# Kernel optimization log

Hardware: AMD Instinct MI355X
Metric: run time of the kernel (lower is better)

## Reference

```python
import jax, jax.numpy as jnp
import numpy as np

B, N, D, V, Y = 4, 2048, 300, 50000, 20000
MAX_REL = 10
LN_EPS = 1e-5


def setup_inputs() -> dict:
    key = jax.random.key(0)
    k1, k2, k3, k4, k5 = jax.random.split(key, 5)
    M_s = jax.random.randint(k1, (B, N), 0, V, dtype=jnp.int64)
    s = 1.0 / np.sqrt(D)
    E_v = jax.random.normal(k2, (V, D), dtype=jnp.float32) * s
    E_v = E_v.at[0].set(0.0)  # padding_idx=0
    E_y = jax.random.normal(k3, (Y, D), dtype=jnp.float32) * s
    E_y = E_y.at[0].set(0.0)
    W_A = jax.random.normal(k4, (D, D), dtype=jnp.float32) * s
    W_O = jax.random.normal(k5, (D, D), dtype=jnp.float32) * s
    gamma = jnp.ones((D,), dtype=jnp.float32)
    beta = jnp.zeros((D,), dtype=jnp.float32)
    return {"M_s": M_s, "E_v": E_v, "E_y": E_y, "W_A": W_A, "W_O": W_O,
            "gamma": gamma, "beta": beta}


def reference(M_s, E_v, E_y, W_A, W_O, gamma, beta):
    # Embedding lookup (dropout is identity in eval / p=0)
    X = E_v[M_s]                                   # [B, N, D]
    Q = X                                          # self-attention mode (v_q=None)
    # weights = Q @ W_A @ X^T
    QW = jnp.einsum('bnd,de->bne', Q, W_A)         # [B, N, D]
    weights = jnp.einsum('bne,bme->bnm', QW, X)    # [B, N, N]
    # relative-distance bias (clipped |i-j|)
    r = jnp.arange(N)
    dist = jnp.clip(jnp.abs(r[None, :] - r[:, None]), 0, MAX_REL).astype(weights.dtype)
    weights = weights - dist
    # padding mask over context (key) positions
    mask = (M_s != 0)                              # [B, N]
    weights = jnp.where(mask[:, None, :], weights, -jnp.inf)
    A = jax.nn.softmax(weights, axis=-1)           # [B, N, N]
    # contextualized query + output projection
    Q_c = jnp.einsum('bnm,bmd->bnd', A, X) @ W_O   # [B, N, D]
    # residual + layernorm over D
    H = Q_c + Q
    mu = jnp.mean(H, axis=-1, keepdims=True)
    var = jnp.mean((H - mu) ** 2, axis=-1, keepdims=True)
    Hn = (H - mu) * jax.lax.rsqrt(var + LN_EPS) * gamma + beta
    # vocab projection over senses
    y_logits = Hn @ E_y.T                          # [B, N, Y]
    return y_logits, A
```

## Files before the change

### kernel.cpp

```cpp
#include <hip/hip_runtime.h>
#include <hip/hip_bf16.h>

#define B_ 4
#define N_ 2048
#define D_ 300
#define Y_ 20000
#define ROWS (B_*N_)

typedef __attribute__((ext_vector_type(8))) short bf16x8;
typedef __attribute__((ext_vector_type(4))) float f32x4;

__device__ __forceinline__ unsigned short f2bf(float f) {
  unsigned u = __float_as_uint(f);
  unsigned r = (u + 0x7FFFu + ((u >> 16) & 1u)) >> 16;
  return (unsigned short)r;
}

__device__ __forceinline__ void gl_lds16(const unsigned short* g, unsigned short* l) {
  __builtin_amdgcn_global_load_lds(
      (const __attribute__((address_space(1))) void*)g,
      (__attribute__((address_space(3))) void*)l, 16, 0, 0);
}

__global__ __launch_bounds__(256) void k_gather_pack(const int* __restrict__ M_s,
    const float* __restrict__ E_v, float* __restrict__ X,
    unsigned short* __restrict__ Xp) {
  __shared__ float xs[320];
  int row = blockIdx.x, tid = threadIdx.x;
  int tok = M_s[row];
  const float* src = E_v + (size_t)tok * D_;
  for (int d = tid; d < 320; d += 256) xs[d] = (d < D_) ? src[d] : 0.f;
  __syncthreads();
  float* dst = X + (size_t)row * D_;
  for (int d = tid; d < D_; d += 256) dst[d] = xs[d];
  if (tid < 40) {
    int kt = tid >> 2, j = tid & 3;
    int tile = row >> 7, fb = (row >> 4) & 7, rl = row & 15;
    unsigned short v[8];
    #pragma unroll
    for (int e = 0; e < 8; ++e) v[e] = f2bf(xs[kt*32 + j*8 + e]);
    size_t off_ = ((size_t)(tile*10 + kt))*4096 + fb*512 + rl*8 + j*128;
    ushort4* o = (ushort4*)&Xp[off_];
    o[0] = make_ushort4(v[0],v[1],v[2],v[3]);
    o[1] = make_ushort4(v[4],v[5],v[6],v[7]);
  }
}

__global__ __launch_bounds__(256) void k_pack(const float* __restrict__ src,
    unsigned short* __restrict__ dst, int nrows, int ncols, int KT) {
  int chunk = blockIdx.x;
  int tile = chunk / KT, kt = chunk - tile*KT;
  size_t obase = (size_t)chunk * 4096;
  #pragma unroll
  for (int p = 0; p < 2; ++p) {
    int idx = p*256 + threadIdx.x;
    int fb = idx >> 6, l = idx & 63;
    int row = tile*128 + fb*16 + (l & 15);
    int gk = kt*32 + (l >> 4)*8;
    unsigned short v[8];
    #pragma unroll
    for (int e = 0; e < 8; ++e) {
      int k = gk + e;
      float f = (row < nrows && k < ncols) ? src[(size_t)row*ncols + k] : 0.f;
      v[e] = f2bf(f);
    }
    ushort4* o = (ushort4*)&dst[obase + (size_t)idx*8];
    o[0] = make_ushort4(v[0],v[1],v[2],v[3]);
    o[1] = make_ushort4(v[4],v[5],v[6],v[7]);
  }
}

__global__ __launch_bounds__(256) void k_packT(const float* __restrict__ src,
    unsigned short* __restrict__ dst, int src_rows, int src_cols, int KT,
    size_t src_bstride, size_t dst_bchunks) {
  __shared__ float ls[32*133];
  int chunk = blockIdx.x, b = blockIdx.y, tid = threadIdx.x;
  const float* s = src + (size_t)b * src_bstride;
  unsigned short* d = dst + ((size_t)b * dst_bchunks + chunk) * 4096;
  int tile = chunk / KT, kt = chunk - tile*KT;
  int c0 = tile*128, k0 = kt*32;
  for (int i = tid; i < 4096; i += 256) {
    int r = i >> 7, c = i & 127;
    int sr = k0 + r, sc = c0 + c;
    ls[r*133 + c] = (sr < src_rows && sc < src_cols) ? s[(size_t)sr*src_cols + sc] : 0.f;
  }
  __syncthreads();
  #pragma unroll
  for (int p = 0; p < 2; ++p) {
    int idx = p*256 + tid;
    int fb = idx >> 6, l = idx & 63;
    int r = fb*16 + (l & 15);
    int kl = (l >> 4)*8;
    unsigned short v[8];
    #pragma unroll
    for (int e = 0; e < 8; ++e) v[e] = f2bf(ls[(kl + e)*133 + r]);
    ushort4* o = (ushort4*)&d[(size_t)idx*8];
    o[0] = make_ushort4(v[0],v[1],v[2],v[3]);
    o[1] = make_ushort4(v[4],v[5],v[6],v[7]);
  }
}

template<int EPI, bool NT, bool PACKOUT, bool SWZ>
__global__ __launch_bounds__(256) void k_gemm10(
    const unsigned short* __restrict__ Ap, const unsigned short* __restrict__ Bp,
    float* __restrict__ out, unsigned short* __restrict__ outp,
    const float* __restrict__ resid, const int* __restrict__ Ms,
    int KTd, int MTB, int NTB, int ncols)
{
  __shared__ __align__(16) union {
    unsigned short bstage[10][4096];
    float epi[64*132];
  } sm;
  int nt, mt, z;
  if (SWZ) {
    int nwg = MTB * NTB;
    int wg = blockIdx.x;
    int cpx = nwg >> 3;
    int swz = (wg & 7) * cpx + (wg >> 3);
    mt = swz % MTB; nt = swz / MTB; z = 0;
  } else {
    nt = blockIdx.x; mt = blockIdx.y; z = blockIdx.z;
  }
  const int tid = threadIdx.x;
  const int wave = tid >> 6, lane = tid & 63;
  const int wm = wave >> 1, wn = wave & 1;
  const unsigned short* Ab = Ap + (size_t)(z*MTB + mt) * 10 * 4096;
  const unsigned short* Bb = Bp + (size_t)(z*NTB + nt) * 10 * 4096;

  #pragma unroll
  for (int kt = 0; kt < 10; ++kt) {
    const unsigned short* gb = Bb + kt*4096 + wave*1024 + lane*8;
    unsigned short* lb = &sm.bstage[kt][wave*1024];
    gl_lds16(gb,       lb);
    gl_lds16(gb + 512, lb + 512);
  }

  const unsigned short* ga = Ab + (wm*4)*512 + lane*8;
  bf16x8 aA[4], aB[4];
  #pragma unroll
  for (int i = 0; i < 4; ++i) aA[i] = *(const bf16x8*)(ga + 0*4096 + i*512);
  #pragma unroll
  for (int i = 0; i < 4; ++i) aB[i] = *(const bf16x8*)(ga + 1*4096 + i*512);

  __syncthreads();

  f32x4 acc[4][4] = {};
  auto mfma_step = [&](int kt, const bf16x8* a) {
    bf16x8 bfr[4];
    #pragma unroll
    for (int i = 0; i < 4; ++i)
      bfr[i] = *(const bf16x8*)&sm.bstage[kt][(wn*4 + i)*512 + lane*8];
    #pragma unroll
    for (int mi = 0; mi < 4; ++mi)
      #pragma unroll
      for (int ni = 0; ni < 4; ++ni)
        acc[mi][ni] = __builtin_amdgcn_mfma_f32_16x16x32_bf16(
            a[mi], bfr[ni], acc[mi][ni], 0, 0, 0);
  };
  auto loadA = [&](int kt, bf16x8* d) {
    #pragma unroll
    for (int i = 0; i < 4; ++i) d[i] = *(const bf16x8*)(ga + kt*4096 + i*512);
  };

  #pragma unroll
  for (int kt = 0; kt < 10; kt += 2) {
    mfma_step(kt, aA);
    if (kt + 2 < 10) loadA(kt + 2, aA);
    mfma_step(kt + 1, aB);
    if (kt + 3 < 10) loadA(kt + 3, aB);
  }

  __syncthreads();

  const int lr0 = (lane >> 4) << 2;
  const int lc0 = wn*64 + (lane & 15);
  const size_t growbase = ((size_t)(z*MTB + mt)) << 7;
  #pragma unroll
  for (int h = 0; h < 2; ++h) {
    if (wm == h) {
      int tok[4];
      if (EPI == 1) {
        #pragma unroll
        for (int ni = 0; ni < 4; ++ni)
          tok[ni] = Ms[z*N_ + (nt<<7) + lc0 + ni*16];
      }
      #pragma unroll
      for (int mi = 0; mi < 4; ++mi) {
        #pragma unroll
        for (int ni = 0; ni < 4; ++ni) {
          int col = lc0 + ni*16;
          #pragma unroll
          for (int r = 0; r < 4; ++r) {
            int row = lr0 + mi*16 + r;
            float v = acc[mi][ni][r];
            if (EPI == 1) {
              int rb = (mt<<7) + h*64 + row;
              int gc = (nt<<7) + col;
              int dd = rb - gc; if (dd < 0) dd = -dd; if (dd > 10) dd = 10;
              v -= (float)dd;
              if (tok[ni] == 0) v = -3.0e38f;
            }
            sm.epi[row*132 + col] = v;
          }
        }
      }
    }
    __syncthreads();
    if (PACKOUT) {
      int prow = tid >> 2, pktq = tid & 3;
      int ktd = nt*4 + pktq;
      if (ktd < KTd) {
        int grl = h*64 + prow;
        int fb = grl >> 4, rl = grl & 15;
        size_t cbase = ((size_t)((z*MTB + mt)*KTd + ktd))*4096 + fb*512 + rl*8;
        #pragma unroll
        for (int oct = 0; oct < 4; ++oct) {
          unsigned short v[8];
          #pragma unroll
          for (int e = 0; e < 8; ++e)
            v[e] = f2bf(sm.epi[prow*132 + pktq*32 + oct*8 + e]);
          ushort4* o = (ushort4*)&outp[cbase + oct*128];
          o[0] = make_ushort4(v[0],v[1],v[2],v[3]);
          o[1] = make_ushort4(v[4],v[5],v[6],v[7]);
        }
      }
    } else {
      const int r0 = tid >> 5;
      const int c4 = (tid & 31) << 2;
      const int gc = (nt << 7) + c4;
      #pragma unroll
      for (int rr = r0; rr < 64; rr += 8) {
        size_t grow = growbase + h*64 + rr;
        if (gc + 3 < ncols) {
          f32x4 v = *(const f32x4*)&sm.epi[rr*132 + c4];
          if (EPI == 2) v += *(const f32x4*)&resid[grow*(size_t)ncols + gc];
          if (NT) __builtin_nontemporal_store(v, (f32x4*)&out[grow*(size_t)ncols + gc]);
          else    *(f32x4*)&out[grow*(size_t)ncols + gc] = v;
        } else {
          #pragma unroll
          for (int e = 0; e < 4; ++e) {
            int c = gc + e;
            if (c < ncols) {
              float v = sm.epi[rr*132 + c4 + e];
              if (EPI == 2) v += resid[grow*(size_t)ncols + c];
              if (NT) __builtin_nontemporal_store(v, &out[grow*(size_t)ncols + c]);
              else    out[grow*(size_t)ncols + c] = v;
            }
          }
        }
      }
    }
    __syncthreads();
  }
}

__global__ __launch_bounds__(256) void k_gemm64(
    const unsigned short* __restrict__ Ap, const unsigned short* __restrict__ Bp,
    unsigned short* __restrict__ outp, int KT, int KTd, int MTB, int NTB)
{
  __shared__ __align__(16) union {
    unsigned short stage[2][2][4096];
    float epi[64*132];
  } sm;
  const int nt = blockIdx.x, mt = blockIdx.y, z = blockIdx.z;
  const int tid = threadIdx.x;
  const int wave = tid >> 6, lane = tid & 63;
  const int wm = wave >> 1, wn = wave & 1;
  const unsigned short* Ab = Ap + (size_t)(z*MTB + mt) * KT * 4096;
  const unsigned short* Bb = Bp + (size_t)(z*NTB + nt) * KT * 4096;
  f32x4 acc[4][4] = {};

  auto stage = [&](int s, int kt) {
    const unsigned short* ga = Ab + kt*4096 + wave*1024 + lane*8;
    const unsigned short* gb = Bb + kt*4096 + wave*1024 + lane*8;
    unsigned short* la = &sm.stage[s][0][wave*1024];
    unsigned short* lb = &sm.stage[s][1][wave*1024];
    gl_lds16(ga,       la);
    gl_lds16(ga + 512, la + 512);
    gl_lds16(gb,       lb);
    gl_lds16(gb + 512, lb + 512);
  };

  stage(0, 0);
  __syncthreads();
  for (int kt = 0; kt < KT; ++kt) {
    int cur = kt & 1;
    if (kt + 1 < KT) stage(cur ^ 1, kt + 1);
    bf16x8 af[4], bfr[4];
    #pragma unroll
    for (int i = 0; i < 4; ++i)
      af[i] = *(const bf16x8*)&sm.stage[cur][0][(wm*4 + i)*512 + lane*8];
    #pragma unroll
    for (int i = 0; i < 4; ++i)
      bfr[i] = *(const bf16x8*)&sm.stage[cur][1][(wn*4 + i)*512 + lane*8];
    #pragma unroll
    for (int mi = 0; mi < 4; ++mi)
      #pragma unroll
      for (int ni = 0; ni < 4; ++ni)
        acc[mi][ni] = __builtin_amdgcn_mfma_f32_16x16x32_bf16(
            af[mi], bfr[ni], acc[mi][ni], 0, 0, 0);
    __syncthreads();
  }

  const int lr0 = (lane >> 4) << 2;
  const int lc0 = wn*64 + (lane & 15);
  #pragma unroll
  for (int h = 0; h < 2; ++h) {
    if (wm == h) {
      #pragma unroll
      for (int mi = 0; mi < 4; ++mi)
        #pragma unroll
        for (int ni = 0; ni < 4; ++ni) {
          int col = lc0 + ni*16;
          #pragma unroll
          for (int r = 0; r < 4; ++r)
            sm.epi[(lr0 + mi*16 + r)*132 + col] = acc[mi][ni][r];
        }
    }
    __syncthreads();
    {
      int prow = tid >> 2, pktq = tid & 3;
      int ktd = nt*4 + pktq;
      if (ktd < KTd) {
        int grl = h*64 + prow;
        int fb = grl >> 4, rl = grl & 15;
        size_t cbase = ((size_t)((z*MTB + mt)*KTd + ktd))*4096 + fb*512 + rl*8;
        #pragma unroll
        for (int oct = 0; oct < 4; ++oct) {
          unsigned short v[8];
          #pragma unroll
          for (int e = 0; e < 8; ++e)
            v[e] = f2bf(sm.epi[prow*132 + pktq*32 + oct*8 + e]);
          ushort4* o = (ushort4*)&outp[cbase + oct*128];
          o[0] = make_ushort4(v[0],v[1],v[2],v[3]);
          o[1] = make_ushort4(v[4],v[5],v[6],v[7]);
        }
      }
    }
    __syncthreads();
  }
}

__global__ __launch_bounds__(256) void k_softmax(float* __restrict__ S,
    unsigned short* __restrict__ Apk) {
  __shared__ float w[N_];
  __shared__ float red[4];
  int row = blockIdx.x, tid = threadIdx.x;
  float* sr = S + (size_t)row * N_;
  float vmax = -3.4e38f;
  for (int m = tid; m < N_; m += 256) { float v = sr[m]; w[m] = v; vmax = fmaxf(vmax, v); }
  #pragma unroll
  for (int off = 32; off; off >>= 1) vmax = fmaxf(vmax, __shfl_down(vmax, off, 64));
  if ((tid & 63) == 0) red[tid >> 6] = vmax;
  __syncthreads();
  vmax = fmaxf(fmaxf(red[0], red[1]), fmaxf(red[2], red[3]));
  float vsum = 0.f;
  for (int m = tid; m < N_; m += 256) {
    float e = __expf(w[m] - vmax);
    w[m] = e;
    vsum += e;
  }
  #pragma unroll
  for (int off = 32; off; off >>= 1) vsum += __shfl_down(vsum, off, 64);
  __syncthreads();
  if ((tid & 63) == 0) red[tid >> 6] = vsum;
  __syncthreads();
  float inv = 1.f / ((red[0] + red[1]) + (red[2] + red[3]));
  for (int m = tid; m < N_; m += 256)
    __builtin_nontemporal_store(w[m] * inv, &sr[m]);
  int kt = tid >> 2, j = tid & 3;
  int m0 = kt*32 + j*8;
  int fb = (row >> 4) & 7, rl = row & 15;
  unsigned short v[8];
  #pragma unroll
  for (int e = 0; e < 8; ++e) v[e] = f2bf(w[m0 + e] * inv);
  size_t off_ = ((size_t)((row >> 7)*64 + kt))*4096 + fb*512 + rl*8 + j*128;
  ushort4* o = (ushort4*)&Apk[off_];
  o[0] = make_ushort4(v[0],v[1],v[2],v[3]);
  o[1] = make_ushort4(v[4],v[5],v[6],v[7]);
}

__global__ __launch_bounds__(320) void k_ln_pack(const float* __restrict__ H,
    const float* __restrict__ gamma, const float* __restrict__ beta,
    unsigned short* __restrict__ Hp) {
  __shared__ float red[5];
  __shared__ float hs[320];
  int row = blockIdx.x, tid = threadIdx.x;
  float h = (tid < D_) ? H[(size_t)row*D_ + tid] : 0.f;
  float s = h;
  #pragma unroll
  for (int off = 32; off; off >>= 1) s += __shfl_down(s, off, 64);
  if ((tid & 63) == 0) red[tid >> 6] = s;
  __syncthreads();
  float mu = (red[0]+red[1]+red[2]+red[3]+red[4]) * (1.f/(float)D_);
  float dv = (tid < D_) ? (h - mu) : 0.f;
  float s2 = dv * dv;
  #pragma unroll
  for (int off = 32; off; off >>= 1) s2 += __shfl_down(s2, off, 64);
  __syncthreads();
  if ((tid & 63) == 0) red[tid >> 6] = s2;
  __syncthreads();
  float var = (red[0]+red[1]+red[2]+red[3]+red[4]) * (1.f/(float)D_);
  float rstd = rsqrtf(var + 1e-5f);
  hs[tid] = (tid < D_) ? (dv * rstd * gamma[tid] + beta[tid]) : 0.f;
  __syncthreads();
  if (tid < 40) {
    int kt = tid >> 2, j = tid & 3;
    int tile = row >> 7, fb = (row >> 4) & 7, rl = row & 15;
    unsigned short v[8];
    #pragma unroll
    for (int e = 0; e < 8; ++e) v[e] = f2bf(hs[kt*32 + j*8 + e]);
    size_t off_ = ((size_t)(tile*10 + kt))*4096 + fb*512 + rl*8 + j*128;
    ushort4* o = (ushort4*)&Hp[off_];
    o[0] = make_ushort4(v[0],v[1],v[2],v[3]);
    o[1] = make_ushort4(v[4],v[5],v[6],v[7]);
  }
}

extern "C" void kernel_launch(void* const* d_in, const int* in_sizes, int n_in,
                              void* d_out, int out_size, void* d_ws, size_t ws_size,
                              hipStream_t stream) {
  const int*   M_s   = (const int*)d_in[0];
  const float* E_v   = (const float*)d_in[1];
  const float* E_y   = (const float*)d_in[2];
  const float* W_A   = (const float*)d_in[3];
  const float* W_O   = (const float*)d_in[4];
  const float* gamma = (const float*)d_in[5];
  const float* beta  = (const float*)d_in[6];

  float* Yl = (float*)d_out;
  float* A  = Yl + (size_t)ROWS * Y_;

  float* X  = (float*)d_ws;
  float* QW = X  + (size_t)ROWS * D_;
  float* H  = QW + (size_t)ROWS * D_;
  unsigned short* Ep = (unsigned short*)(H + (size_t)ROWS * D_);
  unsigned short* Hpk = (unsigned short*)X;

  unsigned short* scr = (unsigned short*)(Yl + 100000000ull);
  unsigned short* Xp  = scr;
  unsigned short* QWp = Xp  + 2621440;
  unsigned short* Wap = QWp + 2621440;
  unsigned short* Wop = Wap + 122880;
  unsigned short* XTp = Wop + 122880;
  unsigned short* Cp  = XTp + 3145728;
  unsigned short* Apk = Cp  + 2621440;

  k_gather_pack<<<ROWS, 256, 0, stream>>>(M_s, E_v, X, Xp);
  k_packT <<<dim3(3*10,1), 256, 0, stream>>>(W_A, Wap, D_, D_, 10, 0, 0);
  k_gemm10<0,false,true,false><<<dim3(3,64,1), 256, 0, stream>>>(
      Xp, Wap, nullptr, QWp, nullptr, nullptr, 10, 64, 3, D_);
  k_gemm10<1,false,false,false><<<dim3(16,16,4), 256, 0, stream>>>(
      QWp, Xp, A, nullptr, nullptr, M_s, 0, 16, 16, N_);
  k_softmax<<<ROWS, 256, 0, stream>>>(A, Apk);
  k_packT <<<dim3(3*64,4), 256, 0, stream>>>(X, XTp, N_, D_, 64, (size_t)N_*D_, 192);
  k_gemm64<<<dim3(3,16,4), 256, 0, stream>>>(Apk, XTp, Cp, 64, 10, 16, 3);
  k_packT <<<dim3(3*10,1), 256, 0, stream>>>(W_O, Wop, D_, D_, 10, 0, 0);
  k_gemm10<2,false,false,false><<<dim3(3,64,1), 256, 0, stream>>>(
      Cp, Wop, H, nullptr, X, nullptr, 0, 64, 3, D_);
  k_ln_pack<<<ROWS, 320, 0, stream>>>(H, gamma, beta, Hpk);
  k_pack  <<<157*10, 256, 0, stream>>>(E_y, Ep, Y_, D_, 10);
  k_gemm10<0,true,false,true><<<dim3(157*64,1,1), 256, 0, stream>>>(
      Hpk, Ep, Yl, nullptr, nullptr, nullptr, 0, 64, 157, Y_);
}
```

Measured before the change: 428.3 us.

## Add 256-row 512-thread GEMM kernel reusing staged B tile for scores and logits

Adds a GEMM kernel in which each 512-thread workgroup computes a 256x128 output tile. The whole K-extent B panel is staged in LDS once and reused across four 64-row sub-blocks, with A fragments read straight from global memory. The attention-score GEMM and the large vocab-logit GEMM both switch to it, halving the number of workgroups and the redundant B loads. The epilogue writes through a 64-row LDS staging buffer four times with extra barriers, and register pressure rises with the 4x4 accumulator tile per wave.

```diff
diff --git a/kernel.cpp b/kernel.cpp
--- a/kernel.cpp
+++ b/kernel.cpp
@@ -97,6 +97,118 @@
     ushort4* o = (ushort4*)&d[(size_t)idx*8];
     o[0] = make_ushort4(v[0],v[1],v[2],v[3]);
     o[1] = make_ushort4(v[4],v[5],v[6],v[7]);
+  }
+}
+
+template<int EPI, bool NT, bool SWZ>
+__global__ __launch_bounds__(512, 4) void k_gemm256(
+    const unsigned short* __restrict__ Ap, const unsigned short* __restrict__ Bp,
+    float* __restrict__ out, const int* __restrict__ Ms,
+    int MTB, int NTB, int ncols)
+{
+  __shared__ __align__(16) union {
+    unsigned short bstage[10][4096];
+    float epi[64*132];
+  } sm;
+  int nt, mt, z;
+  if (SWZ) {
+    int wg = blockIdx.x;
+    int cpx = (MTB*NTB) >> 3;
+    int swz = (wg & 7)*cpx + (wg >> 3);
+    mt = swz % MTB; nt = swz / MTB; z = 0;
+  } else { nt = blockIdx.x; mt = blockIdx.y; z = blockIdx.z; }
+  const int tid = threadIdx.x;
+  const int wave = tid >> 6, lane = tid & 63;
+  const int wm = wave >> 1, wn = wave & 1;
+  const int mtile2 = (z*MTB + mt)*2 + (wm >> 1);
+  const unsigned short* Ab = Ap + (size_t)mtile2 * 10 * 4096;
+  const unsigned short* Bb = Bp + (size_t)(z*NTB + nt) * 10 * 4096;
+
+  #pragma unroll
+  for (int kt = 0; kt < 10; ++kt)
+    gl_lds16(Bb + kt*4096 + wave*512 + lane*8, &sm.bstage[kt][wave*512]);
+
+  const unsigned short* ga = Ab + ((wm & 1)*4)*512 + lane*8;
+  __syncthreads();
+
+  f32x4 acc[4][4] = {};
+  #pragma unroll
+  for (int kt = 0; kt < 10; ++kt) {
+    bf16x8 a4[4], b4[4];
+    #pragma unroll
+    for (int i = 0; i < 4; ++i)
+      a4[i] = *(const bf16x8*)(ga + kt*4096 + i*512);
+    #pragma unroll
+    for (int i = 0; i < 4; ++i)
+      b4[i] = *(const bf16x8*)&sm.bstage[kt][(wn*4 + i)*512 + lane*8];
+    #pragma unroll
+    for (int mi = 0; mi < 4; ++mi)
+      #pragma unroll
+      for (int ni = 0; ni < 4; ++ni)
+        acc[mi][ni] = __builtin_amdgcn_mfma_f32_16x16x32_bf16(
+            a4[mi], b4[ni], acc[mi][ni], 0, 0, 0);
+  }
+  __syncthreads();
+
+  const int lr0 = (lane >> 4) << 2;
+  const int lc0 = wn*64 + (lane & 15);
+  const size_t growbase = ((size_t)(z*MTB + mt)) << 8;
+  #pragma unroll
+  for (int h = 0; h < 4; ++h) {
+    if (wm == h) {
+      int tok[4];
+      if (EPI == 1) {
+        #pragma unroll
+        for (int ni = 0; ni < 4; ++ni)
+          tok[ni] = Ms[z*N_ + (nt<<7) + lc0 + ni*16];
+      }
+      #pragma unroll
+      for (int mi = 0; mi < 4; ++mi) {
+        #pragma unroll
+        for (int ni = 0; ni < 4; ++ni) {
+          int col = lc0 + ni*16;
+          #pragma unroll
+          for (int r = 0; r < 4; ++r) {
+            int row = lr0 + mi*16 + r;
+            float v = acc[mi][ni][r];
+            if (EPI == 1) {
+              int rb = (mt<<8) + h*64 + row;
+              int gc = (nt<<7) + col;
+              int dd = rb - gc; if (dd < 0) dd = -dd; if (dd > 10) dd = 10;
+              v -= (float)dd;
+              if (tok[ni] == 0) v = -3.0e38f;
+            }
+            sm.epi[row*132 + col] = v;
+          }
+        }
+      }
+    }
+    __syncthreads();
+    {
+      const int r0 = tid >> 5;
+      const int c4 = (tid & 31) << 2;
+      const int gc = (nt << 7) + c4;
+      #pragma unroll
+      for (int rr = r0; rr < 64; rr += 16) {
+        size_t grow = growbase + h*64 + rr;
+        if (gc + 3 < ncols) {
+          f32x4 v = *(const f32x4*)&sm.epi[rr*132 + c4];
+          if (NT) __builtin_nontemporal_store(v, (f32x4*)&out[grow*(size_t)ncols + gc]);
+          else    *(f32x4*)&out[grow*(size_t)ncols + gc] = v;
+        } else {
+          #pragma unroll
+          for (int e = 0; e < 4; ++e) {
+            int c = gc + e;
+            if (c < ncols) {
+              float v = sm.epi[rr*132 + c4 + e];
+              if (NT) __builtin_nontemporal_store(v, &out[grow*(size_t)ncols + c]);
+              else    out[grow*(size_t)ncols + c] = v;
+            }
+          }
+        }
+      }
+    }
+    __syncthreads();
   }
 }
 
@@ -450,8 +562,8 @@
   k_packT <<<dim3(3*10,1), 256, 0, stream>>>(W_A, Wap, D_, D_, 10, 0, 0);
   k_gemm10<0,false,true,false><<<dim3(3,64,1), 256, 0, stream>>>(
       Xp, Wap, nullptr, QWp, nullptr, nullptr, 10, 64, 3, D_);
-  k_gemm10<1,false,false,false><<<dim3(16,16,4), 256, 0, stream>>>(
-      QWp, Xp, A, nullptr, nullptr, M_s, 0, 16, 16, N_);
+  k_gemm256<1,false,false><<<dim3(16,8,4), 512, 0, stream>>>(
+      QWp, Xp, A, M_s, 8, 16, N_);
   k_softmax<<<ROWS, 256, 0, stream>>>(A, Apk);
   k_packT <<<dim3(3*64,4), 256, 0, stream>>>(X, XTp, N_, D_, 64, (size_t)N_*D_, 192);
   k_gemm64<<<dim3(3,16,4), 256, 0, stream>>>(Apk, XTp, Cp, 64, 10, 16, 3);
@@ -460,6 +572,6 @@
       Cp, Wop, H, nullptr, X, nullptr, 0, 64, 3, D_);
   k_ln_pack<<<ROWS, 320, 0, stream>>>(H, gamma, beta, Hpk);
   k_pack  <<<157*10, 256, 0, stream>>>(E_y, Ep, Y_, D_, 10);
-  k_gemm10<0,true,false,true><<<dim3(157*64,1,1), 256, 0, stream>>>(
-      Hpk, Ep, Yl, nullptr, nullptr, nullptr, 0, 64, 157, Y_);
-}
+  k_gemm256<0,true,true><<<dim3(157*32,1,1), 512, 0, stream>>>(
+      Hpk, Ep, Yl, nullptr, 32, 157, Y_);
+}
```

Measured after the change: 376.0 us, median of 2. -12.2%, faster.
